# Kernel tuning notes

Measured on AMD Instinct MI355X. Metric: run time of the kernel, lower is better.

## Reference

```python
import jax, jax.numpy as jnp
import numpy as np

THRESHOLD = 0.9  # module buffer _threshold (starting_threshold)


def setup_inputs() -> dict:
    key = jax.random.key(0)
    k_x, k_w = jax.random.split(key)
    B, T, D = 64, 577, 768
    x = jax.random.normal(k_x, (B, T, D), dtype=jnp.float32)
    # nn.Linear(in_dim, 1): weight [1, D] -> stored as vector [D], bias [1]
    w = jax.random.normal(k_w, (D,), dtype=jnp.float32) * (1.0 / np.sqrt(D))
    b = jnp.zeros((1,), dtype=jnp.float32)
    return {"x": x, "w": w, "b": b}


def reference(x, w, b):
    B, T, D = x.shape
    density = int(T * THRESHOLD)  # static: int(577*0.9) = 519
    # head: Linear(D,1) -> sigmoid -> [B, T]  (dropout is identity in eval)
    prob = jax.nn.sigmoid(jnp.einsum('btd,d->bt', x, w) + b[0])
    # keep top-`density` tokens by score (sorted descending, like torch.topk)
    _, top_idx = jax.lax.top_k(prob, density)
    tokens = jnp.take_along_axis(x, top_idx[..., None], axis=1)  # [B, density, D]
    # bottom (T - density) tokens: topk(largest=False) == topk of -prob,
    # which yields values sorted ascending in prob, matching torch
    n_skip = T - density  # 58 > 0
    neg_vals, skip_idx = jax.lax.top_k(-prob, n_skip)
    skip_tokens = jnp.take_along_axis(x, skip_idx[..., None], axis=1)  # [B, n_skip, D]
    weights = jax.nn.softmax(-neg_vals, axis=-1)  # softmax over skipped probs
    summary_token = jnp.sum(skip_tokens * weights[..., None], axis=1, keepdims=True)  # [B,1,D]
    return tokens, skip_tokens, summary_token
```

## Files before the change

kernel.cpp:

```cpp
#include <hip/hip_runtime.h>
#include <math.h>

#define BB 64
#define TT 577
#define DD 768
#define DENS 519
#define NSKIP 58

__device__ inline unsigned long long key_of(double z) {
    long long b = __double_as_longlong(z);
    return (b < 0) ? ~(unsigned long long)b
                   : ((unsigned long long)b | 0x8000000000000000ULL);
}
__device__ inline double key_inv(unsigned long long k) {
    long long b = (k >> 63) ? (long long)(k & 0x7fffffffffffffffULL)
                            : ~(long long)k;
    return __longlong_as_double(b);
}

__global__ __launch_bounds__(256) void k_prob(const float* __restrict__ x,
                                              const float* __restrict__ w,
                                              const float* __restrict__ bias,
                                              unsigned long long* __restrict__ keys,
                                              int nrows) {
    int wave = (int)((blockIdx.x * blockDim.x + threadIdx.x) >> 6);
    int lane = threadIdx.x & 63;
    if (wave >= nrows) return;
    const float4* r4 = (const float4*)(x + (size_t)wave * DD);
    const float4* w4 = (const float4*)w;
    double acc = 0.0;
#pragma unroll
    for (int i = 0; i < 3; ++i) {
        float4 a = r4[lane + 64 * i];
        float4 b = w4[lane + 64 * i];
        acc += (double)a.x * (double)b.x + (double)a.y * (double)b.y
             + (double)a.z * (double)b.z + (double)a.w * (double)b.w;
    }
#pragma unroll
    for (int off = 32; off; off >>= 1)
        acc += __shfl_down(acc, off, 64);
    if (lane == 0) {
        keys[wave] = key_of(acc + (double)bias[0]);
    }
}

__global__ __launch_bounds__(640) void k_rank(const unsigned long long* __restrict__ keys,
                                              int* __restrict__ tok_src,
                                              int* __restrict__ skip_src,
                                              float* __restrict__ skip_w) {
    __shared__ unsigned long long p[TT];
    __shared__ unsigned long long sk[NSKIP];
    int b = blockIdx.x;
    int i = threadIdx.x;
    if (i < TT) p[i] = keys[b * TT + i];
    __syncthreads();
    if (i < TT) {
        unsigned long long ki = p[i];
        int r_desc = 0, r_asc = 0;
#pragma unroll 4
        for (int j = 0; j < TT; ++j) {
            unsigned long long kj = p[j];
            bool tie = (kj == ki) & (j < i);
            r_desc += ((kj > ki) | tie) ? 1 : 0;
            r_asc  += ((kj < ki) | tie) ? 1 : 0;
        }
        if (r_desc < DENS)  tok_src[b * DENS + r_desc] = i;
        if (r_asc < NSKIP) { skip_src[b * NSKIP + r_asc] = i; sk[r_asc] = ki; }
    }
    __syncthreads();
    if (i < 64) {
        double pv = -1.0e300;
        if (i < NSKIP) {
            double z = key_inv(sk[i]);
            pv = 1.0 / (1.0 + exp(-z));
        }
        double m = pv;
#pragma unroll
        for (int off = 32; off; off >>= 1) {
            double o = __shfl_down(m, off, 64);
            m = (o > m) ? o : m;
        }
        m = __shfl(m, 0, 64);
        double e = (i < NSKIP) ? exp(pv - m) : 0.0;
        double s = e;
#pragma unroll
        for (int off = 32; off; off >>= 1)
            s += __shfl_down(s, off, 64);
        s = __shfl(s, 0, 64);
        if (i < NSKIP) skip_w[b * NSKIP + i] = (float)(e / s);
    }
}

__global__ __launch_bounds__(256) void k_gather(const float* __restrict__ x,
                                                const int* __restrict__ tok_src,
                                                const int* __restrict__ skip_src,
                                                float* __restrict__ out) {
    int wave = (int)((blockIdx.x * blockDim.x + threadIdx.x) >> 6);
    int lane = threadIdx.x & 63;
    if (wave >= BB * TT) return;
    int b = wave / TT;
    int k = wave - b * TT;
    int src;
    size_t dst;
    if (k < DENS) {
        src = tok_src[b * DENS + k];
        dst = (size_t)(b * DENS + k) * DD;
    } else {
        int k2 = k - DENS;
        src = skip_src[b * NSKIP + k2];
        dst = (size_t)BB * DENS * DD + (size_t)(b * NSKIP + k2) * DD;
    }
    const float4* s4 = (const float4*)(x + ((size_t)b * TT + src) * DD);
    float4* d4 = (float4*)(out + dst);
#pragma unroll
    for (int i = 0; i < 3; ++i)
        d4[lane + 64 * i] = s4[lane + 64 * i];
}

__global__ __launch_bounds__(256) void k_summary(const float* __restrict__ skip_tok,
                                                 const float* __restrict__ skip_w,
                                                 float* __restrict__ summary) {
    int b = blockIdx.x;
    int t = threadIdx.x;
    float a0 = 0.f, a1 = 0.f, a2 = 0.f;
    for (int k = 0; k < NSKIP; ++k) {
        float wk = skip_w[b * NSKIP + k];
        const float* row = skip_tok + (size_t)(b * NSKIP + k) * DD;
        a0 += wk * row[t];
        a1 += wk * row[t + 256];
        a2 += wk * row[t + 512];
    }
    summary[b * DD + t]       = a0;
    summary[b * DD + t + 256] = a1;
    summary[b * DD + t + 512] = a2;
}

extern "C" void kernel_launch(void* const* d_in, const int* in_sizes, int n_in,
                              void* d_out, int out_size, void* d_ws, size_t ws_size,
                              hipStream_t stream) {
    const float* x    = (const float*)d_in[0];
    const float* w    = (const float*)d_in[1];
    const float* bias = (const float*)d_in[2];
    float* out = (float*)d_out;
    char* ws = (char*)d_ws;

    const int nrows = BB * TT;
    unsigned long long* keys = (unsigned long long*)ws;
    int* tok_src   = (int*)(ws + 295424);
    int* skip_src  = (int*)(ws + 295424 + 132864);
    float* skip_w  = (float*)(ws + 295424 + 132864 + 14848);

    k_prob<<<nrows / 4, 256, 0, stream>>>(x, w, bias, keys, nrows);
    k_rank<<<BB, 640, 0, stream>>>(keys, tok_src, skip_src, skip_w);
    k_gather<<<nrows / 4, 256, 0, stream>>>(x, tok_src, skip_src, out);

    float* skip_tok = out + (size_t)BB * DENS * DD;
    float* summary  = out + (size_t)BB * (DENS + NSKIP) * DD;
    k_summary<<<BB, 256, 0, stream>>>(skip_tok, skip_w, summary);
}
```

Measured before the change: 259.5 us.

## Parallelize ranking per token wave, fuse softmax with summary, nontemporal gather stores

```diff
diff --git a/kernel.cpp b/kernel.cpp
--- a/kernel.cpp
+++ b/kernel.cpp
@@ -6,6 +6,9 @@
 #define DD 768
 #define DENS 519
 #define NSKIP 58
+#define NROWS (BB * TT)
+
+typedef float vf4 __attribute__((ext_vector_type(4)));
 
 __device__ inline unsigned long long key_of(double z) {
     long long b = __double_as_longlong(z);
@@ -21,11 +24,10 @@
 __global__ __launch_bounds__(256) void k_prob(const float* __restrict__ x,
                                               const float* __restrict__ w,
                                               const float* __restrict__ bias,
-                                              unsigned long long* __restrict__ keys,
-                                              int nrows) {
+                                              unsigned long long* __restrict__ keys) {
     int wave = (int)((blockIdx.x * blockDim.x + threadIdx.x) >> 6);
     int lane = threadIdx.x & 63;
-    if (wave >= nrows) return;
+    if (wave >= NROWS) return;
     const float4* r4 = (const float4*)(x + (size_t)wave * DD);
     const float4* w4 = (const float4*)w;
     double acc = 0.0;
@@ -44,34 +46,57 @@
     }
 }
 
-__global__ __launch_bounds__(640) void k_rank(const unsigned long long* __restrict__ keys,
+__global__ __launch_bounds__(256) void k_rank(const unsigned long long* __restrict__ keys,
                                               int* __restrict__ tok_src,
                                               int* __restrict__ skip_src,
-                                              float* __restrict__ skip_w) {
-    __shared__ unsigned long long p[TT];
-    __shared__ unsigned long long sk[NSKIP];
+                                              unsigned long long* __restrict__ skip_key) {
+    int wave = (int)((blockIdx.x * blockDim.x + threadIdx.x) >> 6);
+    int lane = threadIdx.x & 63;
+    if (wave >= NROWS) return;
+    int b = wave / TT;
+    int i = wave - b * TT;
+    const unsigned long long* kb = keys + b * TT;
+    unsigned long long ki = kb[i];
+    int rd = 0, ra = 0;
+#pragma unroll
+    for (int c = 0; c < 10; ++c) {
+        int j = lane + 64 * c;
+        if (j < TT) {
+            unsigned long long kj = kb[j];
+            bool tie = (kj == ki) & (j < i);
+            rd += ((kj > ki) | tie) ? 1 : 0;
+            ra += ((kj < ki) | tie) ? 1 : 0;
+        }
+    }
+    unsigned long long pack = ((unsigned long long)(unsigned)rd << 32) | (unsigned)ra;
+#pragma unroll
+    for (int off = 32; off; off >>= 1)
+        pack += __shfl_down(pack, off, 64);
+    if (lane == 0) {
+        int r_desc = (int)(pack >> 32);
+        int r_asc  = (int)(pack & 0xffffffffu);
+        if (r_desc < DENS) {
+            tok_src[b * DENS + r_desc] = i;
+        } else {
+            skip_src[b * NSKIP + r_asc] = i;
+            skip_key[b * NSKIP + r_asc] = ki;
+        }
+    }
+}
+
+__global__ __launch_bounds__(768) void k_soft(const float* __restrict__ x,
+                                              const int* __restrict__ skip_src,
+                                              const unsigned long long* __restrict__ skip_key,
+                                              float* __restrict__ summary) {
+    __shared__ float wsh[NSKIP];
+    __shared__ int   ssh[NSKIP];
     int b = blockIdx.x;
-    int i = threadIdx.x;
-    if (i < TT) p[i] = keys[b * TT + i];
-    __syncthreads();
-    if (i < TT) {
-        unsigned long long ki = p[i];
-        int r_desc = 0, r_asc = 0;
-#pragma unroll 4
-        for (int j = 0; j < TT; ++j) {
-            unsigned long long kj = p[j];
-            bool tie = (kj == ki) & (j < i);
-            r_desc += ((kj > ki) | tie) ? 1 : 0;
-            r_asc  += ((kj < ki) | tie) ? 1 : 0;
-        }
-        if (r_desc < DENS)  tok_src[b * DENS + r_desc] = i;
-        if (r_asc < NSKIP) { skip_src[b * NSKIP + r_asc] = i; sk[r_asc] = ki; }
-    }
-    __syncthreads();
-    if (i < 64) {
+    int t = threadIdx.x;
+    if (t < NSKIP) ssh[t] = skip_src[b * NSKIP + t];
+    if (t < 64) {
         double pv = -1.0e300;
-        if (i < NSKIP) {
-            double z = key_inv(sk[i]);
+        if (t < NSKIP) {
+            double z = key_inv(skip_key[b * NSKIP + t]);
             pv = 1.0 / (1.0 + exp(-z));
         }
         double m = pv;
@@ -81,14 +106,20 @@
             m = (o > m) ? o : m;
         }
         m = __shfl(m, 0, 64);
-        double e = (i < NSKIP) ? exp(pv - m) : 0.0;
+        double e = (t < NSKIP) ? exp(pv - m) : 0.0;
         double s = e;
 #pragma unroll
         for (int off = 32; off; off >>= 1)
             s += __shfl_down(s, off, 64);
         s = __shfl(s, 0, 64);
-        if (i < NSKIP) skip_w[b * NSKIP + i] = (float)(e / s);
+        if (t < NSKIP) wsh[t] = (float)(e / s);
     }
+    __syncthreads();
+    float acc = 0.f;
+    const float* xb = x + (size_t)b * TT * DD;
+    for (int k = 0; k < NSKIP; ++k)
+        acc += wsh[k] * xb[(size_t)ssh[k] * DD + t];
+    summary[(size_t)b * DD + t] = acc;
 }
 
 __global__ __launch_bounds__(256) void k_gather(const float* __restrict__ x,
@@ -97,7 +128,7 @@
                                                 float* __restrict__ out) {
     int wave = (int)((blockIdx.x * blockDim.x + threadIdx.x) >> 6);
     int lane = threadIdx.x & 63;
-    if (wave >= BB * TT) return;
+    if (wave >= NROWS) return;
     int b = wave / TT;
     int k = wave - b * TT;
     int src;
@@ -110,29 +141,13 @@
         src = skip_src[b * NSKIP + k2];
         dst = (size_t)BB * DENS * DD + (size_t)(b * NSKIP + k2) * DD;
     }
-    const float4* s4 = (const float4*)(x + ((size_t)b * TT + src) * DD);
-    float4* d4 = (float4*)(out + dst);
+    const vf4* s4 = (const vf4*)(x + ((size_t)b * TT + src) * DD);
+    vf4* d4 = (vf4*)(out + dst);
 #pragma unroll
-    for (int i = 0; i < 3; ++i)
-        d4[lane + 64 * i] = s4[lane + 64 * i];
-}
-
-__global__ __launch_bounds__(256) void k_summary(const float* __restrict__ skip_tok,
-                                                 const float* __restrict__ skip_w,
-                                                 float* __restrict__ summary) {
-    int b = blockIdx.x;
-    int t = threadIdx.x;
-    float a0 = 0.f, a1 = 0.f, a2 = 0.f;
-    for (int k = 0; k < NSKIP; ++k) {
-        float wk = skip_w[b * NSKIP + k];
-        const float* row = skip_tok + (size_t)(b * NSKIP + k) * DD;
-        a0 += wk * row[t];
-        a1 += wk * row[t + 256];
-        a2 += wk * row[t + 512];
+    for (int i = 0; i < 3; ++i) {
+        vf4 v = s4[lane + 64 * i];
+        __builtin_nontemporal_store(v, &d4[lane + 64 * i]);
     }
-    summary[b * DD + t]       = a0;
-    summary[b * DD + t + 256] = a1;
-    summary[b * DD + t + 512] = a2;
 }
 
 extern "C" void kernel_launch(void* const* d_in, const int* in_sizes, int n_in,
@@ -144,17 +159,17 @@
     float* out = (float*)d_out;
     char* ws = (char*)d_ws;
 
-    const int nrows = BB * TT;
     unsigned long long* keys = (unsigned long long*)ws;
-    int* tok_src   = (int*)(ws + 295424);
-    int* skip_src  = (int*)(ws + 295424 + 132864);
-    float* skip_w  = (float*)(ws + 295424 + 132864 + 14848);
+    int* tok_src  = (int*)(ws + 295424);
+    int* skip_src = (int*)(ws + 295424 + 132864);
+    unsigned long long* skip_key =
+        (unsigned long long*)(ws + 295424 + 132864 + 14848);
 
-    k_prob<<<nrows / 4, 256, 0, stream>>>(x, w, bias, keys, nrows);
-    k_rank<<<BB, 640, 0, stream>>>(keys, tok_src, skip_src, skip_w);
-    k_gather<<<nrows / 4, 256, 0, stream>>>(x, tok_src, skip_src, out);
+    const int nblk = NROWS / 4;
 
-    float* skip_tok = out + (size_t)BB * DENS * DD;
-    float* summary  = out + (size_t)BB * (DENS + NSKIP) * DD;
-    k_summary<<<BB, 256, 0, stream>>>(skip_tok, skip_w, summary);
+    k_prob<<<nblk, 256, 0, stream>>>(x, w, bias, keys);
+    k_rank<<<nblk, 256, 0, stream>>>(keys, tok_src, skip_src, skip_key);
+    k_soft<<<BB, 768, 0, stream>>>(x, skip_src, skip_key,
+                                   out + (size_t)BB * (DENS + NSKIP) * DD);
+    k_gather<<<nblk, 256, 0, stream>>>(x, tok_src, skip_src, out);
 }
```

Result: faster. 241.1 us (-7.1%).
